# Optimization experiments

Hardware: AMD Instinct MI355X
Metric: run time of the kernel (lower is better)

Reference implementation:

```python
import jax, jax.numpy as jnp
import numpy as np

N, E, D, H = 100000, 1600000, 128, 128


def setup_inputs() -> dict:
    key = jax.random.key(0)
    ks = jax.random.split(key, 7)
    x = jax.random.normal(ks[0], (N, D), dtype=jnp.float32)
    edge_index = jax.random.randint(ks[1], (2, E), 0, N, dtype=jnp.int64)
    edge_weight = jax.random.uniform(ks[2], (E,), dtype=jnp.float32)
    s = 1.0 / np.sqrt(D)
    W0 = jax.random.normal(ks[3], (D, H), dtype=jnp.float32) * s
    b0 = jnp.zeros((H,), dtype=jnp.float32)
    W1 = jax.random.normal(ks[4], (H, H), dtype=jnp.float32) * (1.0 / np.sqrt(H))
    b1 = jnp.zeros((H,), dtype=jnp.float32)
    return {"x": x, "edge_weight": edge_weight, "W0": W0, "b0": b0,
            "W1": W1, "b1": b1, "edge_index": edge_index}


def reference(x, edge_weight, W0, b0, W1, b1, edge_index):
    src, dst = edge_index[0], edge_index[1]
    n = x.shape[0]
    # gcn_norm with self-loops (fill_value=1): deg includes the self-loop weight
    deg = jax.ops.segment_sum(edge_weight, dst, num_segments=n) + 1.0  # [N]
    dis = jnp.where(deg > 0, jax.lax.rsqrt(deg), 0.0)                  # deg^-1/2
    norm = dis[src] * edge_weight * dis[dst]                           # [E]
    self_coef = dis * dis                                              # self-loop norm = 1/deg

    def gcn_layer(h, W, b):
        hW = h @ W                                                     # [N,H]
        agg = jax.ops.segment_sum(norm[:, None] * hW[src], dst, num_segments=n)
        agg = agg + self_coef[:, None] * hW                            # self-loop term
        return jax.nn.relu(agg + b)

    h1 = gcn_layer(x, W0, b0)
    h2 = gcn_layer(h1, W1, b1)
    return jnp.concatenate([h1, h2], axis=1)  # [N, 2H]
```

## Files before the change

### kernel.cpp

```cpp
#include <hip/hip_runtime.h>
#include <hip/hip_fp16.h>


typedef unsigned int u32;
typedef _Float16 f16;
typedef f16 f16x8 __attribute__((ext_vector_type(8)));
typedef float f32x4 __attribute__((ext_vector_type(4)));

__global__ __launch_bounds__(256) void k_wfrag(const float* __restrict__ W0,
                                               const float* __restrict__ W1,
                                               __half* __restrict__ Wf) {
    int idx = blockIdx.x * 256 + threadIdx.x;
    const float* W = (idx < 2048) ? W0 : W1;
    int id = idx & 2047;
    int l = id & 63, nt = (id >> 6) & 7, ks = id >> 9;
    int nn = nt * 16 + (l & 15);
    int kb = ks * 32 + ((l >> 4) & 3) * 4;
    union { int4 v; __half h[8]; } pk;
#pragma unroll
    for (int j = 0; j < 8; ++j) {
        int k = kb + (j & 3) + 16 * (j >> 2);
        pk.h[j] = __float2half(W[k * 128 + nn]);
    }
    *(int4*)(Wf + (size_t)idx * 8) = pk.v;
}

__global__ __launch_bounds__(256) void k_p1(const int* __restrict__ dst,
                                            u32* __restrict__ H,
                                            int e, int NB, int nch) {
    __shared__ u32 lcnt[512];
    const int t = threadIdx.x, bid = blockIdx.x;
    lcnt[t] = 0; lcnt[t + 256] = 0;
    __syncthreads();
    int i0 = bid * 4096 + t;
#pragma unroll
    for (int u = 0; u < 16; ++u) {
        int i = i0 + u * 256;
        if (i < e) atomicAdd(&lcnt[(u32)dst[i] >> 9], 1u);
    }
    __syncthreads();
    for (int b = t; b < NB; b += 256) H[(size_t)b * nch + bid] = lcnt[b];
}

__global__ __launch_bounds__(256) void k_scan1(u32* data, u32* sums, int n) {
    __shared__ u32 tmp[256];
    int gid = blockIdx.x * 256 + threadIdx.x;
    u32 v = (gid < n) ? data[gid] : 0;
    tmp[threadIdx.x] = v;
    __syncthreads();
    for (int off = 1; off < 256; off <<= 1) {
        u32 t = (threadIdx.x >= off) ? tmp[threadIdx.x - off] : 0;
        __syncthreads();
        tmp[threadIdx.x] += t;
        __syncthreads();
    }
    if (gid < n) data[gid] = tmp[threadIdx.x] - v;
    if (threadIdx.x == 255) sums[blockIdx.x] = tmp[255];
}

__global__ __launch_bounds__(512) void k_scan2(u32* sums, int nb) {
    __shared__ u32 tmp[512];
    u32 v = (threadIdx.x < nb) ? sums[threadIdx.x] : 0;
    tmp[threadIdx.x] = v;
    __syncthreads();
    for (int off = 1; off < 512; off <<= 1) {
        u32 t = (threadIdx.x >= off) ? tmp[threadIdx.x - off] : 0;
        __syncthreads();
        tmp[threadIdx.x] += t;
        __syncthreads();
    }
    if (threadIdx.x < nb) sums[threadIdx.x] = tmp[threadIdx.x] - v;
}

__global__ __launch_bounds__(256) void k_scan3(u32* data, const u32* sums, int n) {
    int gid = blockIdx.x * 256 + threadIdx.x;
    if (gid < n) data[gid] += sums[blockIdx.x];
}

__global__ __launch_bounds__(256) void k_p2(const int* __restrict__ src,
                                            const int* __restrict__ dst,
                                            const float* __restrict__ w,
                                            const u32* __restrict__ H,
                                            int2* __restrict__ tmp,
                                            int e, int NB, int nch) {
    __shared__ u32 lcnt[512];
    __shared__ u32 lbase[512];
    const int t = threadIdx.x, bid = blockIdx.x;
    lcnt[t] = 0; lcnt[t + 256] = 0;
    __syncthreads();
    for (int b = t; b < NB; b += 256) lbase[b] = H[(size_t)b * nch + bid];
    __syncthreads();
    int i0 = bid * 4096 + t;
#pragma unroll
    for (int u = 0; u < 16; ++u) {
        int i = i0 + u * 256;
        if (i < e) {
            int d = dst[i];
            u32 b = (u32)d >> 9;
            u32 lr = atomicAdd(&lcnt[b], 1u);
            tmp[lbase[b] + lr] = make_int2(src[i] | ((d & 511) << 17),
                                           __float_as_int(w[i]));
        }
    }
}

__device__ __forceinline__ void gemm_body(const float* __restrict__ A, int lda,
                                          const __half* __restrict__ Wf,
                                          __half* __restrict__ C, int n,
                                          int bid, int t) {
    const int w2 = t >> 6, l = t & 63;
    const int node = bid * 64 + w2 * 16 + (l & 15);
    const int koff = ((l >> 4) & 3) * 4;
    const bool ok = node < n;
    const float* ap = A + (size_t)(ok ? node : 0) * lda;

    f16x8 af[4];
#pragma unroll
    for (int ks = 0; ks < 4; ++ks) {
        float4 a0 = make_float4(0.f, 0.f, 0.f, 0.f), a1 = a0;
        if (ok) {
            a0 = *(const float4*)(ap + ks * 32 + koff);
            a1 = *(const float4*)(ap + ks * 32 + koff + 16);
        }
        f16x8 h;
        h[0] = (f16)a0.x; h[1] = (f16)a0.y; h[2] = (f16)a0.z; h[3] = (f16)a0.w;
        h[4] = (f16)a1.x; h[5] = (f16)a1.y; h[6] = (f16)a1.z; h[7] = (f16)a1.w;
        af[ks] = h;
    }

    f32x4 acc[8];
#pragma unroll
    for (int i = 0; i < 8; ++i) acc[i] = (f32x4){0.f, 0.f, 0.f, 0.f};

#pragma unroll
    for (int ks = 0; ks < 4; ++ks) {
#pragma unroll
        for (int nt = 0; nt < 8; ++nt) {
            f16x8 wf = *(const f16x8*)(Wf + ((size_t)(ks * 8 + nt) * 64 + l) * 8);
            acc[nt] = __builtin_amdgcn_mfma_f32_16x16x32_f16(wf, af[ks], acc[nt], 0, 0, 0);
        }
    }

    if (ok) {
        const int c0 = ((l >> 4) & 3) * 4;
#pragma unroll
        for (int nt = 0; nt < 8; ++nt) {
            union { short4 s4; __half h[4]; } pk;
#pragma unroll
            for (int r2 = 0; r2 < 4; ++r2) pk.h[r2] = __float2half(acc[nt][r2]);
            *(short4*)(C + (size_t)node * 128 + nt * 16 + c0) = pk.s4;
        }
    }
}

__global__ __launch_bounds__(512) void k_p3(const int2* __restrict__ tmp,
                                            const u32* __restrict__ H,
                                            int2* __restrict__ ep,
                                            int* __restrict__ rowstart,
                                            float* __restrict__ dis,
                                            int e, int n, int NB, int nch,
                                            const float* __restrict__ A, int lda,
                                            const __half* __restrict__ Wf,
                                            __half* __restrict__ C) {
    const int bid = blockIdx.x, t = threadIdx.x;
    if (bid >= NB) {
        int g = bid - NB;
        gemm_body(A, lda, Wf, C, n, g * 2 + (t >> 8), t & 255);
        return;
    }
    __shared__ u32 cnt[512];
    __shared__ u32 degx[512];
    __shared__ u32 off[512];
    __shared__ u32 stmp[512];

    cnt[t] = 0; degx[t] = 0;
    __syncthreads();

    const int bs = (int)H[(size_t)bid * nch];
    const int be = (bid + 1 < NB) ? (int)H[(size_t)(bid + 1) * nch] : e;

    for (int j = bs + t; j < be; j += 512) {
        int2 r = tmp[j];
        u32 low = ((u32)r.x >> 17) & 511u;
        atomicAdd(&cnt[low], 1u);
        atomicAdd(&degx[low], (u32)(__int_as_float(r.y) * 1048576.0f + 0.5f));
    }
    __syncthreads();

    u32 v = cnt[t];
    stmp[t] = v;
    __syncthreads();
    for (int o = 1; o < 512; o <<= 1) {
        u32 x = (t >= o) ? stmp[t - o] : 0u;
        __syncthreads();
        stmp[t] += x;
        __syncthreads();
    }
    off[t] = stmp[t] - v;

    const int node = bid * 512 + t;
    if (node < n) {
        rowstart[node] = bs + (int)off[t];
        dis[node] = rsqrtf(1.0f + (float)degx[t] * (1.0f / 1048576.0f));
    }
    __syncthreads();

    for (int j = bs + t; j < be; j += 512) {
        int2 r = tmp[j];
        u32 low = ((u32)r.x >> 17) & 511u;
        u32 p = atomicAdd(&off[low], 1u);
        ep[bs + p] = make_int2(r.x & 0x1FFFF, r.y);
    }
}

__global__ __launch_bounds__(256) void k_gemm(const float* __restrict__ A, int lda,
                                              const __half* __restrict__ Wf,
                                              __half* __restrict__ C, int n) {
    gemm_body(A, lda, Wf, C, n, blockIdx.x, threadIdx.x);
}

__global__ __launch_bounds__(256) void k_agg(const __half* __restrict__ hW,
                                             const int2* __restrict__ ep,
                                             const int* __restrict__ rowstart,
                                             const float* __restrict__ dis,
                                             const float* __restrict__ bias,
                                             float* __restrict__ outcol,
                                             int n, int e) {
    int wid = blockIdx.x * 4 + (threadIdx.x >> 6);
    int lane = threadIdx.x & 63;
    if (wid >= n) return;

    int start = rowstart[wid];
    int end   = (wid == n - 1) ? e : rowstart[wid + 1];
    start = __builtin_amdgcn_readfirstlane(start);
    end   = __builtin_amdgcn_readfirstlane(end);

    float dd = dis[wid];
    float2 h = __half22float2(*(const __half2*)(hW + (size_t)wid * 128 + lane * 2));
    float2 acc;
    acc.x = dd * dd * h.x;
    acc.y = dd * dd * h.y;

    int j = start;
    for (; j + 15 < end; j += 16) {
        int2 r[16];
        float ds[16];
        __half2 v[16];
#pragma unroll
        for (int u = 0; u < 16; ++u) r[u] = ep[j + u];
#pragma unroll
        for (int u = 0; u < 16; ++u) ds[u] = dis[r[u].x];
#pragma unroll
        for (int u = 0; u < 16; ++u)
            v[u] = *(const __half2*)(hW + (size_t)r[u].x * 128 + lane * 2);
#pragma unroll
        for (int u = 0; u < 16; ++u) {
            float nm = ds[u] * __int_as_float(r[u].y) * dd;
            float2 f = __half22float2(v[u]);
            acc.x += nm * f.x;
            acc.y += nm * f.y;
        }
    }
    for (; j + 7 < end; j += 8) {
        int2 r[8];
        float ds[8];
        __half2 v[8];
#pragma unroll
        for (int u = 0; u < 8; ++u) r[u] = ep[j + u];
#pragma unroll
        for (int u = 0; u < 8; ++u) ds[u] = dis[r[u].x];
#pragma unroll
        for (int u = 0; u < 8; ++u)
            v[u] = *(const __half2*)(hW + (size_t)r[u].x * 128 + lane * 2);
#pragma unroll
        for (int u = 0; u < 8; ++u) {
            float nm = ds[u] * __int_as_float(r[u].y) * dd;
            float2 f = __half22float2(v[u]);
            acc.x += nm * f.x;
            acc.y += nm * f.y;
        }
    }
    for (; j + 3 < end; j += 4) {
        int2 r[4];
        float ds[4];
        __half2 v[4];
#pragma unroll
        for (int u = 0; u < 4; ++u) r[u] = ep[j + u];
#pragma unroll
        for (int u = 0; u < 4; ++u) ds[u] = dis[r[u].x];
#pragma unroll
        for (int u = 0; u < 4; ++u)
            v[u] = *(const __half2*)(hW + (size_t)r[u].x * 128 + lane * 2);
#pragma unroll
        for (int u = 0; u < 4; ++u) {
            float nm = ds[u] * __int_as_float(r[u].y) * dd;
            float2 f = __half22float2(v[u]);
            acc.x += nm * f.x;
            acc.y += nm * f.y;
        }
    }
    for (; j < end; ++j) {
        int2 rec = ep[j];
        float nm = dis[rec.x] * __int_as_float(rec.y) * dd;
        float2 v = __half22float2(*(const __half2*)(hW + (size_t)rec.x * 128 + lane * 2));
        acc.x += nm * v.x;
        acc.y += nm * v.y;
    }

    float2 b = *(const float2*)(bias + lane * 2);
    float2 o;
    o.x = fmaxf(acc.x + b.x, 0.f);
    o.y = fmaxf(acc.y + b.y, 0.f);
    *(float2*)(outcol + (size_t)wid * 256 + lane * 2) = o;
}

extern "C" void kernel_launch(void* const* d_in, const int* in_sizes, int n_in,
                              void* d_out, int out_size, void* d_ws, size_t ws_size,
                              hipStream_t stream) {
    const float* x  = (const float*)d_in[0];
    const float* ew = (const float*)d_in[1];
    const float* W0 = (const float*)d_in[2];
    const float* b0 = (const float*)d_in[3];
    const float* W1 = (const float*)d_in[4];
    const float* b1 = (const float*)d_in[5];
    const int*   ei = (const int*)d_in[6];

    const int N = in_sizes[0] / 128;
    const int E = in_sizes[1];
    const int* src = ei;
    const int* dst = ei + E;
    float* out = (float*)d_out;

    const int NB  = (N + 511) >> 9;
    const int nch = (E + 4095) >> 12;
    const int scanN = NB * nch;
    const int scanB = (scanN + 255) / 256;
    const int gT = (N + 63) / 64;
    const int gemmB = (gT + 1) / 2;
    const int gA = (N + 3) / 4;

    const size_t Hsz = (size_t)((scanN + 1) & ~1);
    const size_t Npad = (size_t)((N + 1) & ~1);
    u32*   H        = (u32*)d_ws;
    int*   rowstart = (int*)(H + Hsz);
    float* dis      = (float*)(rowstart + Npad);
    int2*  tmp      = (int2*)(dis + Npad);
    int2*  ep       = tmp + E;
    __half* hW      = (__half*)(ep + E);
    __half* Wf      = hW + (size_t)N * 128;
    u32*   sums     = (u32*)(Wf + 32768);

    k_wfrag<<<16, 256, 0, stream>>>(W0, W1, Wf);
    k_p1<<<nch, 256, 0, stream>>>(dst, H, E, NB, nch);
    k_scan1<<<scanB, 256, 0, stream>>>(H, sums, scanN);
    k_scan2<<<1, 512, 0, stream>>>(sums, scanB);
    k_scan3<<<scanB, 256, 0, stream>>>(H, sums, scanN);
    k_p2<<<nch, 256, 0, stream>>>(src, dst, ew, H, tmp, E, NB, nch);
    k_p3<<<NB + gemmB, 512, 0, stream>>>(tmp, H, ep, rowstart, dis, E, N, NB, nch,
                                         x, 128, Wf, hW);

    k_agg<<<gA, 256, 0, stream>>>(hW, ep, rowstart, dis, b0, out, N, E);

    k_gemm<<<gT, 256, 0, stream>>>(out, 256, Wf + 16384, hW, N);
    k_agg<<<gA, 256, 0, stream>>>(hW, ep, rowstart, dis, b1, out + 128, N, E);
}
```

Before: 269.4 us.

## Prescale hW by deg^-1/2 in GEMM and split aggregation across half-waves

The GEMM epilogue now multiplies each output row by dis[node], so the aggregation no longer gathers dis[src] for every edge and applies dd once at the end. k_agg is restructured so each half-wave handles alternate edges with 4-wide fp16 loads, and the two halves are combined with a shuffle, doubling edge-level parallelism per wave. The first-layer GEMM is un-fused from k_p3 and launched separately because it now depends on dis, which gives up the earlier overlap of the GEMM with CSR construction.

```diff
diff --git a/kernel.cpp b/kernel.cpp
--- a/kernel.cpp
+++ b/kernel.cpp
@@ -4,6 +4,7 @@
 
 typedef unsigned int u32;
 typedef _Float16 f16;
+typedef f16 f16x4 __attribute__((ext_vector_type(4)));
 typedef f16 f16x8 __attribute__((ext_vector_type(8)));
 typedef float f32x4 __attribute__((ext_vector_type(4)));
 
@@ -104,12 +105,65 @@
     }
 }
 
-__device__ __forceinline__ void gemm_body(const float* __restrict__ A, int lda,
-                                          const __half* __restrict__ Wf,
-                                          __half* __restrict__ C, int n,
-                                          int bid, int t) {
+__global__ __launch_bounds__(512) void k_p3(const int2* __restrict__ tmp,
+                                            const u32* __restrict__ H,
+                                            int2* __restrict__ ep,
+                                            int* __restrict__ rowstart,
+                                            float* __restrict__ dis,
+                                            int e, int n, int NB, int nch) {
+    const int bid = blockIdx.x, t = threadIdx.x;
+    __shared__ u32 cnt[512];
+    __shared__ u32 degx[512];
+    __shared__ u32 off[512];
+    __shared__ u32 stmp[512];
+
+    cnt[t] = 0; degx[t] = 0;
+    __syncthreads();
+
+    const int bs = (int)H[(size_t)bid * nch];
+    const int be = (bid + 1 < NB) ? (int)H[(size_t)(bid + 1) * nch] : e;
+
+    for (int j = bs + t; j < be; j += 512) {
+        int2 r = tmp[j];
+        u32 low = ((u32)r.x >> 17) & 511u;
+        atomicAdd(&cnt[low], 1u);
+        atomicAdd(&degx[low], (u32)(__int_as_float(r.y) * 1048576.0f + 0.5f));
+    }
+    __syncthreads();
+
+    u32 v = cnt[t];
+    stmp[t] = v;
+    __syncthreads();
+    for (int o = 1; o < 512; o <<= 1) {
+        u32 x = (t >= o) ? stmp[t - o] : 0u;
+        __syncthreads();
+        stmp[t] += x;
+        __syncthreads();
+    }
+    off[t] = stmp[t] - v;
+
+    const int node = bid * 512 + t;
+    if (node < n) {
+        rowstart[node] = bs + (int)off[t];
+        dis[node] = rsqrtf(1.0f + (float)degx[t] * (1.0f / 1048576.0f));
+    }
+    __syncthreads();
+
+    for (int j = bs + t; j < be; j += 512) {
+        int2 r = tmp[j];
+        u32 low = ((u32)r.x >> 17) & 511u;
+        u32 p = atomicAdd(&off[low], 1u);
+        ep[bs + p] = make_int2(r.x & 0x1FFFF, r.y);
+    }
+}
+
+__global__ __launch_bounds__(256) void k_gemm(const float* __restrict__ A, int lda,
+                                              const __half* __restrict__ Wf,
+                                              __half* __restrict__ C,
+                                              const float* __restrict__ dis, int n) {
+    const int t = threadIdx.x;
     const int w2 = t >> 6, l = t & 63;
-    const int node = bid * 64 + w2 * 16 + (l & 15);
+    const int node = blockIdx.x * 64 + w2 * 16 + (l & 15);
     const int koff = ((l >> 4) & 3) * 4;
     const bool ok = node < n;
     const float* ap = A + (size_t)(ok ? node : 0) * lda;
@@ -142,84 +196,20 @@
     }
 
     if (ok) {
+        const float ds = dis[node];
         const int c0 = ((l >> 4) & 3) * 4;
 #pragma unroll
         for (int nt = 0; nt < 8; ++nt) {
             union { short4 s4; __half h[4]; } pk;
 #pragma unroll
-            for (int r2 = 0; r2 < 4; ++r2) pk.h[r2] = __float2half(acc[nt][r2]);
+            for (int r2 = 0; r2 < 4; ++r2)
+                pk.h[r2] = __float2half(acc[nt][r2] * ds);
             *(short4*)(C + (size_t)node * 128 + nt * 16 + c0) = pk.s4;
         }
     }
 }
 
-__global__ __launch_bounds__(512) void k_p3(const int2* __restrict__ tmp,
-                                            const u32* __restrict__ H,
-                                            int2* __restrict__ ep,
-                                            int* __restrict__ rowstart,
-                                            float* __restrict__ dis,
-                                            int e, int n, int NB, int nch,
-                                            const float* __restrict__ A, int lda,
-                                            const __half* __restrict__ Wf,
-                                            __half* __restrict__ C) {
-    const int bid = blockIdx.x, t = threadIdx.x;
-    if (bid >= NB) {
-        int g = bid - NB;
-        gemm_body(A, lda, Wf, C, n, g * 2 + (t >> 8), t & 255);
-        return;
-    }
-    __shared__ u32 cnt[512];
-    __shared__ u32 degx[512];
-    __shared__ u32 off[512];
-    __shared__ u32 stmp[512];
-
-    cnt[t] = 0; degx[t] = 0;
-    __syncthreads();
-
-    const int bs = (int)H[(size_t)bid * nch];
-    const int be = (bid + 1 < NB) ? (int)H[(size_t)(bid + 1) * nch] : e;
-
-    for (int j = bs + t; j < be; j += 512) {
-        int2 r = tmp[j];
-        u32 low = ((u32)r.x >> 17) & 511u;
-        atomicAdd(&cnt[low], 1u);
-        atomicAdd(&degx[low], (u32)(__int_as_float(r.y) * 1048576.0f + 0.5f));
-    }
-    __syncthreads();
-
-    u32 v = cnt[t];
-    stmp[t] = v;
-    __syncthreads();
-    for (int o = 1; o < 512; o <<= 1) {
-        u32 x = (t >= o) ? stmp[t - o] : 0u;
-        __syncthreads();
-        stmp[t] += x;
-        __syncthreads();
-    }
-    off[t] = stmp[t] - v;
-
-    const int node = bid * 512 + t;
-    if (node < n) {
-        rowstart[node] = bs + (int)off[t];
-        dis[node] = rsqrtf(1.0f + (float)degx[t] * (1.0f / 1048576.0f));
-    }
-    __syncthreads();
-
-    for (int j = bs + t; j < be; j += 512) {
-        int2 r = tmp[j];
-        u32 low = ((u32)r.x >> 17) & 511u;
-        u32 p = atomicAdd(&off[low], 1u);
-        ep[bs + p] = make_int2(r.x & 0x1FFFF, r.y);
-    }
-}
-
-__global__ __launch_bounds__(256) void k_gemm(const float* __restrict__ A, int lda,
-                                              const __half* __restrict__ Wf,
-                                              __half* __restrict__ C, int n) {
-    gemm_body(A, lda, Wf, C, n, blockIdx.x, threadIdx.x);
-}
-
-__global__ __launch_bounds__(256) void k_agg(const __half* __restrict__ hW,
+__global__ __launch_bounds__(256) void k_agg(const __half* __restrict__ hWh,
                                              const int2* __restrict__ ep,
                                              const int* __restrict__ rowstart,
                                              const float* __restrict__ dis,
@@ -229,89 +219,65 @@
     int wid = blockIdx.x * 4 + (threadIdx.x >> 6);
     int lane = threadIdx.x & 63;
     if (wid >= n) return;
+    const int half = lane >> 5, sl = lane & 31;
+    const f16* hW = (const f16*)hWh;
 
     int start = rowstart[wid];
     int end   = (wid == n - 1) ? e : rowstart[wid + 1];
     start = __builtin_amdgcn_readfirstlane(start);
     end   = __builtin_amdgcn_readfirstlane(end);
 
-    float dd = dis[wid];
-    float2 h = __half22float2(*(const __half2*)(hW + (size_t)wid * 128 + lane * 2));
-    float2 acc;
-    acc.x = dd * dd * h.x;
-    acc.y = dd * dd * h.y;
-
-    int j = start;
-    for (; j + 15 < end; j += 16) {
-        int2 r[16];
-        float ds[16];
-        __half2 v[16];
-#pragma unroll
-        for (int u = 0; u < 16; ++u) r[u] = ep[j + u];
-#pragma unroll
-        for (int u = 0; u < 16; ++u) ds[u] = dis[r[u].x];
-#pragma unroll
-        for (int u = 0; u < 16; ++u)
-            v[u] = *(const __half2*)(hW + (size_t)r[u].x * 128 + lane * 2);
-#pragma unroll
-        for (int u = 0; u < 16; ++u) {
-            float nm = ds[u] * __int_as_float(r[u].y) * dd;
-            float2 f = __half22float2(v[u]);
-            acc.x += nm * f.x;
-            acc.y += nm * f.y;
-        }
-    }
-    for (; j + 7 < end; j += 8) {
-        int2 r[8];
-        float ds[8];
-        __half2 v[8];
-#pragma unroll
-        for (int u = 0; u < 8; ++u) r[u] = ep[j + u];
-#pragma unroll
-        for (int u = 0; u < 8; ++u) ds[u] = dis[r[u].x];
-#pragma unroll
-        for (int u = 0; u < 8; ++u)
-            v[u] = *(const __half2*)(hW + (size_t)r[u].x * 128 + lane * 2);
-#pragma unroll
-        for (int u = 0; u < 8; ++u) {
-            float nm = ds[u] * __int_as_float(r[u].y) * dd;
-            float2 f = __half22float2(v[u]);
-            acc.x += nm * f.x;
-            acc.y += nm * f.y;
-        }
-    }
-    for (; j + 3 < end; j += 4) {
-        int2 r[4];
-        float ds[4];
-        __half2 v[4];
-#pragma unroll
-        for (int u = 0; u < 4; ++u) r[u] = ep[j + u];
-#pragma unroll
-        for (int u = 0; u < 4; ++u) ds[u] = dis[r[u].x];
-#pragma unroll
-        for (int u = 0; u < 4; ++u)
-            v[u] = *(const __half2*)(hW + (size_t)r[u].x * 128 + lane * 2);
-#pragma unroll
-        for (int u = 0; u < 4; ++u) {
-            float nm = ds[u] * __int_as_float(r[u].y) * dd;
-            float2 f = __half22float2(v[u]);
-            acc.x += nm * f.x;
-            acc.y += nm * f.y;
-        }
-    }
-    for (; j < end; ++j) {
-        int2 rec = ep[j];
-        float nm = dis[rec.x] * __int_as_float(rec.y) * dd;
-        float2 v = __half22float2(*(const __half2*)(hW + (size_t)rec.x * 128 + lane * 2));
-        acc.x += nm * v.x;
-        acc.y += nm * v.y;
-    }
-
-    float2 b = *(const float2*)(bias + lane * 2);
-    float2 o;
-    o.x = fmaxf(acc.x + b.x, 0.f);
-    o.y = fmaxf(acc.y + b.y, 0.f);
-    *(float2*)(outcol + (size_t)wid * 256 + lane * 2) = o;
+    const float dd = dis[wid];
+
+    f16x4 hv = *(const f16x4*)(hW + (size_t)wid * 128 + sl * 4);
+    float a0 = 0.f, a1 = 0.f, a2 = 0.f, a3 = 0.f;
+    if (half == 0) {
+        a0 = (float)hv[0]; a1 = (float)hv[1];
+        a2 = (float)hv[2]; a3 = (float)hv[3];
+    }
+
+    int jb = start;
+    for (; jb + 7 < end; jb += 8) {
+        int2 r0 = ep[jb + half];
+        int2 r1 = ep[jb + 2 + half];
+        int2 r2 = ep[jb + 4 + half];
+        int2 r3 = ep[jb + 6 + half];
+        f16x4 v0 = *(const f16x4*)(hW + (size_t)r0.x * 128 + sl * 4);
+        f16x4 v1 = *(const f16x4*)(hW + (size_t)r1.x * 128 + sl * 4);
+        f16x4 v2 = *(const f16x4*)(hW + (size_t)r2.x * 128 + sl * 4);
+        f16x4 v3 = *(const f16x4*)(hW + (size_t)r3.x * 128 + sl * 4);
+        float n0 = __int_as_float(r0.y), n1 = __int_as_float(r1.y);
+        float n2 = __int_as_float(r2.y), n3 = __int_as_float(r3.y);
+        a0 += n0 * (float)v0[0] + n1 * (float)v1[0] + n2 * (float)v2[0] + n3 * (float)v3[0];
+        a1 += n0 * (float)v0[1] + n1 * (float)v1[1] + n2 * (float)v2[1] + n3 * (float)v3[1];
+        a2 += n0 * (float)v0[2] + n1 * (float)v1[2] + n2 * (float)v2[2] + n3 * (float)v3[2];
+        a3 += n0 * (float)v0[3] + n1 * (float)v1[3] + n2 * (float)v2[3] + n3 * (float)v3[3];
+    }
+    for (; jb < end; jb += 2) {
+        int idx = jb + half;
+        int2 r = (idx < end) ? ep[idx] : make_int2(wid, 0);
+        f16x4 v = *(const f16x4*)(hW + (size_t)r.x * 128 + sl * 4);
+        float nm = __int_as_float(r.y);
+        a0 += nm * (float)v[0];
+        a1 += nm * (float)v[1];
+        a2 += nm * (float)v[2];
+        a3 += nm * (float)v[3];
+    }
+
+    a0 += __shfl_xor(a0, 32);
+    a1 += __shfl_xor(a1, 32);
+    a2 += __shfl_xor(a2, 32);
+    a3 += __shfl_xor(a3, 32);
+
+    if (half == 0) {
+        float4 b = *(const float4*)(bias + sl * 4);
+        float4 o;
+        o.x = fmaxf(dd * a0 + b.x, 0.f);
+        o.y = fmaxf(dd * a1 + b.y, 0.f);
+        o.z = fmaxf(dd * a2 + b.z, 0.f);
+        o.w = fmaxf(dd * a3 + b.w, 0.f);
+        *(float4*)(outcol + (size_t)wid * 256 + sl * 4) = o;
+    }
 }
 
 extern "C" void kernel_launch(void* const* d_in, const int* in_sizes, int n_in,
@@ -336,7 +302,6 @@
     const int scanN = NB * nch;
     const int scanB = (scanN + 255) / 256;
     const int gT = (N + 63) / 64;
-    const int gemmB = (gT + 1) / 2;
     const int gA = (N + 3) / 4;
 
     const size_t Hsz = (size_t)((scanN + 1) & ~1);
@@ -356,11 +321,11 @@
     k_scan2<<<1, 512, 0, stream>>>(sums, scanB);
     k_scan3<<<scanB, 256, 0, stream>>>(H, sums, scanN);
     k_p2<<<nch, 256, 0, stream>>>(src, dst, ew, H, tmp, E, NB, nch);
-    k_p3<<<NB + gemmB, 512, 0, stream>>>(tmp, H, ep, rowstart, dis, E, N, NB, nch,
-                                         x, 128, Wf, hW);
-
+    k_p3<<<NB, 512, 0, stream>>>(tmp, H, ep, rowstart, dis, E, N, NB, nch);
+
+    k_gemm<<<gT, 256, 0, stream>>>(x, 128, Wf, hW, dis, N);
     k_agg<<<gA, 256, 0, stream>>>(hW, ep, rowstart, dis, b0, out, N, E);
 
-    k_gemm<<<gT, 256, 0, stream>>>(out, 256, Wf + 16384, hW, N);
+    k_gemm<<<gT, 256, 0, stream>>>(out, 256, Wf + 16384, hW, dis, N);
     k_agg<<<gA, 256, 0, stream>>>(hW, ep, rowstart, dis, b1, out + 128, N, E);
 }
```

Measured after the change: 281.0 us. 4.3% more time.

## Fold source-side normalization into edge weights and move first GEMM into count kernel

Applied to the files above, without the earlier changes.

The CSR build is split into two kernels: one computes row starts and deg^-1/2, and a second scatters edges with weight pre-multiplied by dis[src]. The aggregation kernels then no longer gather dis per edge and apply the destination factor once per row. The first-layer GEMM moves from the CSR-build kernel into the histogram kernel so it overlaps with counting. This adds one kernel launch and a second pass over the tmp buffer, in exchange for removing a random gather per edge in both aggregation layers.

```diff
diff --git a/kernel.cpp b/kernel.cpp
--- a/kernel.cpp
+++ b/kernel.cpp
@@ -25,11 +25,67 @@
     *(int4*)(Wf + (size_t)idx * 8) = pk.v;
 }
 
-__global__ __launch_bounds__(256) void k_p1(const int* __restrict__ dst,
-                                            u32* __restrict__ H,
-                                            int e, int NB, int nch) {
+__device__ __forceinline__ void gemm_body(const float* __restrict__ A, int lda,
+                                          const __half* __restrict__ Wf,
+                                          __half* __restrict__ C, int n,
+                                          int bid, int t) {
+    const int w2 = t >> 6, l = t & 63;
+    const int node = bid * 64 + w2 * 16 + (l & 15);
+    const int koff = ((l >> 4) & 3) * 4;
+    const bool ok = node < n;
+    const float* ap = A + (size_t)(ok ? node : 0) * lda;
+
+    f16x8 af[4];
+#pragma unroll
+    for (int ks = 0; ks < 4; ++ks) {
+        float4 a0 = make_float4(0.f, 0.f, 0.f, 0.f), a1 = a0;
+        if (ok) {
+            a0 = *(const float4*)(ap + ks * 32 + koff);
+            a1 = *(const float4*)(ap + ks * 32 + koff + 16);
+        }
+        f16x8 h;
+        h[0] = (f16)a0.x; h[1] = (f16)a0.y; h[2] = (f16)a0.z; h[3] = (f16)a0.w;
+        h[4] = (f16)a1.x; h[5] = (f16)a1.y; h[6] = (f16)a1.z; h[7] = (f16)a1.w;
+        af[ks] = h;
+    }
+
+    f32x4 acc[8];
+#pragma unroll
+    for (int i = 0; i < 8; ++i) acc[i] = (f32x4){0.f, 0.f, 0.f, 0.f};
+
+#pragma unroll
+    for (int ks = 0; ks < 4; ++ks) {
+#pragma unroll
+        for (int nt = 0; nt < 8; ++nt) {
+            f16x8 wf = *(const f16x8*)(Wf + ((size_t)(ks * 8 + nt) * 64 + l) * 8);
+            acc[nt] = __builtin_amdgcn_mfma_f32_16x16x32_f16(wf, af[ks], acc[nt], 0, 0, 0);
+        }
+    }
+
+    if (ok) {
+        const int c0 = ((l >> 4) & 3) * 4;
+#pragma unroll
+        for (int nt = 0; nt < 8; ++nt) {
+            union { short4 s4; __half h[4]; } pk;
+#pragma unroll
+            for (int r2 = 0; r2 < 4; ++r2) pk.h[r2] = __float2half(acc[nt][r2]);
+            *(short4*)(C + (size_t)node * 128 + nt * 16 + c0) = pk.s4;
+        }
+    }
+}
+
+__global__ __launch_bounds__(256) void k_p1gemm(const int* __restrict__ dst,
+                                                u32* __restrict__ H,
+                                                int e, int NB, int nch,
+                                                const float* __restrict__ A, int lda,
+                                                const __half* __restrict__ Wf,
+                                                __half* __restrict__ C, int n) {
+    const int bid = blockIdx.x, t = threadIdx.x;
+    if (bid >= nch) {
+        gemm_body(A, lda, Wf, C, n, bid - nch, t);
+        return;
+    }
     __shared__ u32 lcnt[512];
-    const int t = threadIdx.x, bid = blockIdx.x;
     lcnt[t] = 0; lcnt[t + 256] = 0;
     __syncthreads();
     int i0 = bid * 4096 + t;
@@ -104,73 +160,14 @@
     }
 }
 
-__device__ __forceinline__ void gemm_body(const float* __restrict__ A, int lda,
-                                          const __half* __restrict__ Wf,
-                                          __half* __restrict__ C, int n,
-                                          int bid, int t) {
-    const int w2 = t >> 6, l = t & 63;
-    const int node = bid * 64 + w2 * 16 + (l & 15);
-    const int koff = ((l >> 4) & 3) * 4;
-    const bool ok = node < n;
-    const float* ap = A + (size_t)(ok ? node : 0) * lda;
-
-    f16x8 af[4];
-#pragma unroll
-    for (int ks = 0; ks < 4; ++ks) {
-        float4 a0 = make_float4(0.f, 0.f, 0.f, 0.f), a1 = a0;
-        if (ok) {
-            a0 = *(const float4*)(ap + ks * 32 + koff);
-            a1 = *(const float4*)(ap + ks * 32 + koff + 16);
-        }
-        f16x8 h;
-        h[0] = (f16)a0.x; h[1] = (f16)a0.y; h[2] = (f16)a0.z; h[3] = (f16)a0.w;
-        h[4] = (f16)a1.x; h[5] = (f16)a1.y; h[6] = (f16)a1.z; h[7] = (f16)a1.w;
-        af[ks] = h;
-    }
-
-    f32x4 acc[8];
-#pragma unroll
-    for (int i = 0; i < 8; ++i) acc[i] = (f32x4){0.f, 0.f, 0.f, 0.f};
-
-#pragma unroll
-    for (int ks = 0; ks < 4; ++ks) {
-#pragma unroll
-        for (int nt = 0; nt < 8; ++nt) {
-            f16x8 wf = *(const f16x8*)(Wf + ((size_t)(ks * 8 + nt) * 64 + l) * 8);
-            acc[nt] = __builtin_amdgcn_mfma_f32_16x16x32_f16(wf, af[ks], acc[nt], 0, 0, 0);
-        }
-    }
-
-    if (ok) {
-        const int c0 = ((l >> 4) & 3) * 4;
-#pragma unroll
-        for (int nt = 0; nt < 8; ++nt) {
-            union { short4 s4; __half h[4]; } pk;
-#pragma unroll
-            for (int r2 = 0; r2 < 4; ++r2) pk.h[r2] = __float2half(acc[nt][r2]);
-            *(short4*)(C + (size_t)node * 128 + nt * 16 + c0) = pk.s4;
-        }
-    }
-}
-
-__global__ __launch_bounds__(512) void k_p3(const int2* __restrict__ tmp,
-                                            const u32* __restrict__ H,
-                                            int2* __restrict__ ep,
-                                            int* __restrict__ rowstart,
-                                            float* __restrict__ dis,
-                                            int e, int n, int NB, int nch,
-                                            const float* __restrict__ A, int lda,
-                                            const __half* __restrict__ Wf,
-                                            __half* __restrict__ C) {
+__global__ __launch_bounds__(512) void k_p3a(const int2* __restrict__ tmp,
+                                             const u32* __restrict__ H,
+                                             int* __restrict__ rowstart,
+                                             float* __restrict__ dis,
+                                             int e, int n, int NB, int nch) {
     const int bid = blockIdx.x, t = threadIdx.x;
-    if (bid >= NB) {
-        int g = bid - NB;
-        gemm_body(A, lda, Wf, C, n, g * 2 + (t >> 8), t & 255);
-        return;
-    }
     __shared__ u32 cnt[512];
     __shared__ u32 degx[512];
-    __shared__ u32 off[512];
     __shared__ u32 stmp[512];
 
     cnt[t] = 0; degx[t] = 0;
@@ -196,20 +193,36 @@
         stmp[t] += x;
         __syncthreads();
     }
-    off[t] = stmp[t] - v;
 
     const int node = bid * 512 + t;
     if (node < n) {
-        rowstart[node] = bs + (int)off[t];
+        rowstart[node] = bs + (int)(stmp[t] - v);
         dis[node] = rsqrtf(1.0f + (float)degx[t] * (1.0f / 1048576.0f));
     }
-    __syncthreads();
+}
+
+__global__ __launch_bounds__(512) void k_p3b(const int2* __restrict__ tmp,
+                                             const u32* __restrict__ H,
+                                             const int* __restrict__ rowstart,
+                                             const float* __restrict__ dis,
+                                             int2* __restrict__ ep,
+                                             int e, int n, int NB, int nch) {
+    const int bid = blockIdx.x, t = threadIdx.x;
+    __shared__ u32 cur[512];
+    const int node = bid * 512 + t;
+    cur[t] = (node < n) ? (u32)rowstart[node] : 0u;
+    __syncthreads();
+
+    const int bs = (int)H[(size_t)bid * nch];
+    const int be = (bid + 1 < NB) ? (int)H[(size_t)(bid + 1) * nch] : e;
 
     for (int j = bs + t; j < be; j += 512) {
         int2 r = tmp[j];
         u32 low = ((u32)r.x >> 17) & 511u;
-        u32 p = atomicAdd(&off[low], 1u);
-        ep[bs + p] = make_int2(r.x & 0x1FFFF, r.y);
+        int s = r.x & 0x1FFFF;
+        float wd = __int_as_float(r.y) * dis[s];
+        u32 p = atomicAdd(&cur[low], 1u);
+        ep[p] = make_int2(s, __float_as_int(wd));
     }
 }
 
@@ -235,27 +248,24 @@
     start = __builtin_amdgcn_readfirstlane(start);
     end   = __builtin_amdgcn_readfirstlane(end);
 
-    float dd = dis[wid];
+    const float dd = dis[wid];
     float2 h = __half22float2(*(const __half2*)(hW + (size_t)wid * 128 + lane * 2));
     float2 acc;
-    acc.x = dd * dd * h.x;
-    acc.y = dd * dd * h.y;
+    acc.x = dd * h.x;
+    acc.y = dd * h.y;
 
     int j = start;
     for (; j + 15 < end; j += 16) {
         int2 r[16];
-        float ds[16];
         __half2 v[16];
 #pragma unroll
         for (int u = 0; u < 16; ++u) r[u] = ep[j + u];
-#pragma unroll
-        for (int u = 0; u < 16; ++u) ds[u] = dis[r[u].x];
 #pragma unroll
         for (int u = 0; u < 16; ++u)
             v[u] = *(const __half2*)(hW + (size_t)r[u].x * 128 + lane * 2);
 #pragma unroll
         for (int u = 0; u < 16; ++u) {
-            float nm = ds[u] * __int_as_float(r[u].y) * dd;
+            float nm = __int_as_float(r[u].y);
             float2 f = __half22float2(v[u]);
             acc.x += nm * f.x;
             acc.y += nm * f.y;
@@ -263,18 +273,15 @@
     }
     for (; j + 7 < end; j += 8) {
         int2 r[8];
-        float ds[8];
         __half2 v[8];
 #pragma unroll
         for (int u = 0; u < 8; ++u) r[u] = ep[j + u];
-#pragma unroll
-        for (int u = 0; u < 8; ++u) ds[u] = dis[r[u].x];
 #pragma unroll
         for (int u = 0; u < 8; ++u)
             v[u] = *(const __half2*)(hW + (size_t)r[u].x * 128 + lane * 2);
 #pragma unroll
         for (int u = 0; u < 8; ++u) {
-            float nm = ds[u] * __int_as_float(r[u].y) * dd;
+            float nm = __int_as_float(r[u].y);
             float2 f = __half22float2(v[u]);
             acc.x += nm * f.x;
             acc.y += nm * f.y;
@@ -282,18 +289,15 @@
     }
     for (; j + 3 < end; j += 4) {
         int2 r[4];
-        float ds[4];
         __half2 v[4];
 #pragma unroll
         for (int u = 0; u < 4; ++u) r[u] = ep[j + u];
-#pragma unroll
-        for (int u = 0; u < 4; ++u) ds[u] = dis[r[u].x];
 #pragma unroll
         for (int u = 0; u < 4; ++u)
             v[u] = *(const __half2*)(hW + (size_t)r[u].x * 128 + lane * 2);
 #pragma unroll
         for (int u = 0; u < 4; ++u) {
-            float nm = ds[u] * __int_as_float(r[u].y) * dd;
+            float nm = __int_as_float(r[u].y);
             float2 f = __half22float2(v[u]);
             acc.x += nm * f.x;
             acc.y += nm * f.y;
@@ -301,7 +305,7 @@
     }
     for (; j < end; ++j) {
         int2 rec = ep[j];
-        float nm = dis[rec.x] * __int_as_float(rec.y) * dd;
+        float nm = __int_as_float(rec.y);
         float2 v = __half22float2(*(const __half2*)(hW + (size_t)rec.x * 128 + lane * 2));
         acc.x += nm * v.x;
         acc.y += nm * v.y;
@@ -309,8 +313,8 @@
 
     float2 b = *(const float2*)(bias + lane * 2);
     float2 o;
-    o.x = fmaxf(acc.x + b.x, 0.f);
-    o.y = fmaxf(acc.y + b.y, 0.f);
+    o.x = fmaxf(dd * acc.x + b.x, 0.f);
+    o.y = fmaxf(dd * acc.y + b.y, 0.f);
     *(float2*)(outcol + (size_t)wid * 256 + lane * 2) = o;
 }
 
@@ -336,7 +340,6 @@
     const int scanN = NB * nch;
     const int scanB = (scanN + 255) / 256;
     const int gT = (N + 63) / 64;
-    const int gemmB = (gT + 1) / 2;
     const int gA = (N + 3) / 4;
 
     const size_t Hsz = (size_t)((scanN + 1) & ~1);
@@ -351,13 +354,13 @@
     u32*   sums     = (u32*)(Wf + 32768);
 
     k_wfrag<<<16, 256, 0, stream>>>(W0, W1, Wf);
-    k_p1<<<nch, 256, 0, stream>>>(dst, H, E, NB, nch);
+    k_p1gemm<<<nch + gT, 256, 0, stream>>>(dst, H, E, NB, nch, x, 128, Wf, hW, N);
     k_scan1<<<scanB, 256, 0, stream>>>(H, sums, scanN);
     k_scan2<<<1, 512, 0, stream>>>(sums, scanB);
     k_scan3<<<scanB, 256, 0, stream>>>(H, sums, scanN);
     k_p2<<<nch, 256, 0, stream>>>(src, dst, ew, H, tmp, E, NB, nch);
-    k_p3<<<NB + gemmB, 512, 0, stream>>>(tmp, H, ep, rowstart, dis, E, N, NB, nch,
-                                         x, 128, Wf, hW);
+    k_p3a<<<NB, 512, 0, stream>>>(tmp, H, rowstart, dis, E, N, NB, nch);
+    k_p3b<<<NB, 512, 0, stream>>>(tmp, H, rowstart, dis, ep, E, N, NB, nch);
 
     k_agg<<<gA, 256, 0, stream>>>(hW, ep, rowstart, dis, b0, out, N, E);
 
```

Result: no change. 272.3 us (+1.1%).
